# Performance work log

Measured on AMD Instinct MI355X. Metric: run time of the kernel, lower is better.

Reference implementation:

```python
import jax, jax.numpy as jnp
import numpy as np

N = 50000      # num nodes
E = 800000     # num edges (avg degree 16)
IN_FEA = 256
OU_FEA = 64


def setup_inputs() -> dict:
    key = jax.random.key(0)
    k_h, k_w, k_r, k_c, k_v = jax.random.split(key, 5)
    h = jax.random.normal(k_h, (N, IN_FEA), dtype=jnp.float32)
    # Linear(in_fea, ou_fea, bias=None): weight applied as h @ W, W [IN, OUT]
    W = jax.random.normal(k_w, (IN_FEA, OU_FEA), dtype=jnp.float32) / np.sqrt(IN_FEA)
    row = jax.random.randint(k_r, (E,), 0, N, dtype=jnp.int32)
    col = jax.random.randint(k_c, (E,), 0, N, dtype=jnp.int32)
    vals = jax.random.uniform(k_v, (E,), dtype=jnp.float32)
    return {"h": h, "W": W, "row": row, "col": col, "vals": vals}


def reference(h, W, row, col, vals):
    # dense projection: [N, IN] @ [IN, OUT] -> [N, OUT]
    hp = h @ W
    # torch builds sparse tensor with indices [col, row], i.e. G = A^T,
    # so torch.sparse.mm(G, hp)[i] = sum over edges with col==i of vals * hp[row]
    msg = hp[row] * vals[:, None]                      # [E, OUT] gather + scale
    out = jax.ops.segment_sum(msg, col, num_segments=N)  # scatter-add to dest
    return out
```

## Files before the change

### kernel.cpp

```cpp
#include <hip/hip_runtime.h>
#include <hip/hip_bf16.h>

#define IN_F 256
#define OU_F 64
#define BKN 128
#define BSHIFT 7
#define CHUNK 4096
#define STAGE_CAP 4096

typedef __attribute__((ext_vector_type(8))) short short8;
typedef __attribute__((ext_vector_type(4))) float f32x4;

__device__ inline short8 cvt8(float4 a, float4 b)
{
    union { short8 s8; __hip_bfloat162 h2[4]; } u;
    u.h2[0] = __float22bfloat162_rn(make_float2(a.x, a.y));
    u.h2[1] = __float22bfloat162_rn(make_float2(a.z, a.w));
    u.h2[2] = __float22bfloat162_rn(make_float2(b.x, b.y));
    u.h2[3] = __float22bfloat162_rn(make_float2(b.z, b.w));
    return u.s8;
}

__global__ void __launch_bounds__(256, 4)
gemm_mfma_kernel(const float* __restrict__ h, const float* __restrict__ W,
                 float* __restrict__ hp, int N)
{
    __shared__ unsigned short Wt[64][264];
    const int t = threadIdx.x;

#pragma unroll
    for (int i = 0; i < 32; ++i) {
        int p  = t + i * 256;
        int c  = p & 63;
        int k0 = (p >> 6) << 1;
        float x = W[(size_t)k0 * OU_F + c];
        float y = W[(size_t)(k0 + 1) * OU_F + c];
        __hip_bfloat162 bb = __float22bfloat162_rn(make_float2(x, y));
        *reinterpret_cast<unsigned*>(&Wt[c][k0]) = *reinterpret_cast<unsigned*>(&bb);
    }
    __syncthreads();

    const int l    = t & 63;
    const int wv   = t >> 6;
    const int cl   = l & 15;
    const int kg   = l >> 4;
    const int rbase = blockIdx.x * 64 + wv * 16;
    const int r    = rbase + cl;
    const int rld  = min(r, N - 1);
    const float4* hrow = reinterpret_cast<const float4*>(h) + (size_t)rld * (IN_F / 4);

    f32x4 acc[4];
#pragma unroll
    for (int nt = 0; nt < 4; ++nt) acc[nt] = (f32x4){0.f, 0.f, 0.f, 0.f};

#pragma unroll
    for (int ks = 0; ks < 8; ++ks) {
        float4 a0 = hrow[ks * 8 + kg * 2];
        float4 a1 = hrow[ks * 8 + kg * 2 + 1];
        short8 af = cvt8(a0, a1);
#pragma unroll
        for (int nt = 0; nt < 4; ++nt) {
            short8 bf = *reinterpret_cast<const short8*>(&Wt[nt * 16 + cl][ks * 32 + kg * 8]);
            acc[nt] = __builtin_amdgcn_mfma_f32_16x16x32_bf16(af, bf, acc[nt], 0, 0, 0);
        }
    }

#pragma unroll
    for (int nt = 0; nt < 4; ++nt)
#pragma unroll
        for (int rg = 0; rg < 4; ++rg) {
            int rr = rbase + kg * 4 + rg;
            if (rr < N)
                hp[(size_t)rr * OU_F + nt * 16 + cl] = acc[nt][rg];
        }
}

__global__ void __launch_bounds__(256)
hist_kernel(const int* __restrict__ col, int* __restrict__ bcnt, int E, int NB)
{
    __shared__ int lh[512];
    const int t = threadIdx.x;
    lh[t] = 0; lh[t + 256] = 0;
    __syncthreads();
    const int n4 = E >> 2;
    const int4* c4 = (const int4*)col;
    for (int i = blockIdx.x * 256 + t; i < n4; i += gridDim.x * 256) {
        int4 v = c4[i];
        atomicAdd(&lh[v.x >> BSHIFT], 1);
        atomicAdd(&lh[v.y >> BSHIFT], 1);
        atomicAdd(&lh[v.z >> BSHIFT], 1);
        atomicAdd(&lh[v.w >> BSHIFT], 1);
    }
    if (blockIdx.x == 0)
        for (int e = (n4 << 2) + t; e < E; e += 256)
            atomicAdd(&lh[col[e] >> BSHIFT], 1);
    __syncthreads();
    for (int i = t; i < NB; i += 256)
        if (lh[i]) atomicAdd(&bcnt[i], lh[i]);
}

__global__ void __launch_bounds__(256)
scan_kernel(const int* __restrict__ bcnt, int* __restrict__ boffs,
            int* __restrict__ bcursor, int NB)
{
    __shared__ int c[512];
    __shared__ int s[256];
    const int t = threadIdx.x;
    c[t]       = (t < NB)       ? bcnt[t] : 0;
    c[t + 256] = (t + 256 < NB) ? bcnt[t + 256] : 0;
    __syncthreads();
    s[t] = c[2 * t] + c[2 * t + 1];
    __syncthreads();
    for (int d = 1; d < 256; d <<= 1) {
        int v = (t >= d) ? s[t - d] : 0;
        __syncthreads();
        s[t] += v;
        __syncthreads();
    }
    int excl = (t > 0) ? s[t - 1] : 0;
    int e0 = excl;
    int e1 = excl + c[2 * t];
    if (2 * t < NB)     { boffs[2 * t]     = e0; bcursor[2 * t]     = e0; }
    if (2 * t + 1 < NB) { boffs[2 * t + 1] = e1; bcursor[2 * t + 1] = e1; }
    if (t == 255) boffs[NB] = s[255];
}

__global__ void __launch_bounds__(256)
partition_kernel(const int* __restrict__ row, const int* __restrict__ col,
                 const float* __restrict__ vals, int* __restrict__ bcursor,
                 int2* __restrict__ epk, int E, int NB)
{
    __shared__ int  hist[512];
    __shared__ int  X[512];
    __shared__ int  gshift[512];
    __shared__ int  s[256];
    __shared__ int2 stage[CHUNK];
    __shared__ int  gpos[CHUNK];

    const int t = threadIdx.x;
    const int base = blockIdx.x * CHUNK;
    const int n = min(CHUNK, E - base);

    hist[t] = 0; hist[t + 256] = 0;
    __syncthreads();

#pragma unroll
    for (int k = 0; k < 16; ++k) {
        int i = t + k * 256;
        if (i < n) atomicAdd(&hist[col[base + i] >> BSHIFT], 1);
    }
    __syncthreads();

    s[t] = hist[2 * t] + hist[2 * t + 1];
    __syncthreads();
    for (int d = 1; d < 256; d <<= 1) {
        int v = (t >= d) ? s[t - d] : 0;
        __syncthreads();
        s[t] += v;
        __syncthreads();
    }
    int excl = (t > 0) ? s[t - 1] : 0;
    X[2 * t]     = excl;
    X[2 * t + 1] = excl + hist[2 * t];
    __syncthreads();

    for (int i = t; i < NB; i += 256) {
        int hcnt = hist[i];
        int g = hcnt ? atomicAdd(&bcursor[i], hcnt) : 0;
        gshift[i] = g - X[i];
    }
    __syncthreads();

#pragma unroll
    for (int k = 0; k < 16; ++k) {
        int i = t + k * 256;
        if (i < n) {
            int e  = base + i;
            int cv = col[e];
            int b  = cv >> BSHIFT;
            int r  = atomicAdd(&X[b], 1);
            unsigned pk = (unsigned)row[e] | ((unsigned)(cv & (BKN - 1)) << 17);
            stage[r] = make_int2((int)pk, __float_as_int(vals[e]));
            gpos[r]  = gshift[b] + r;
        }
    }
    __syncthreads();

#pragma unroll
    for (int k = 0; k < 16; ++k) {
        int i = t + k * 256;
        if (i < n) epk[gpos[i]] = stage[i];
    }
}

__global__ void __launch_bounds__(256)
csr_kernel(const int2* __restrict__ epk, const int* __restrict__ boffs,
           int2* __restrict__ epk2, int* __restrict__ node_offs,
           int N, int NB)
{
    __shared__ int  cnt[BKN];
    __shared__ int  sc[BKN];
    __shared__ int  cur[BKN];
    __shared__ int2 stage[STAGE_CAP];
    const int t = threadIdx.x;
    const int b = blockIdx.x;
    const int s = boffs[b], e = boffs[b + 1];
    const int n = e - s;
    const int node0 = b << BSHIFT;

    if (t < BKN) cnt[t] = 0;
    __syncthreads();
    for (int i = t; i < n; i += 256)
        atomicAdd(&cnt[((unsigned)epk[s + i].x) >> 17], 1);
    __syncthreads();

    if (t < BKN) sc[t] = cnt[t];
    __syncthreads();
    for (int d = 1; d < BKN; d <<= 1) {
        int v = 0;
        if (t < BKN && t >= d) v = sc[t - d];
        __syncthreads();
        if (t < BKN) sc[t] += v;
        __syncthreads();
    }
    if (t < BKN) {
        int excl = sc[t] - cnt[t];
        cur[t] = excl;
        int node = node0 + t;
        if (node < N) node_offs[node] = s + excl;
    }
    if (b == NB - 1 && t == 0) node_offs[N] = e;
    __syncthreads();

    if (n <= STAGE_CAP) {
        for (int i = t; i < n; i += 256) {
            int2 r = epk[s + i];
            int pos = atomicAdd(&cur[((unsigned)r.x) >> 17], 1);
            stage[pos] = r;
        }
        __syncthreads();
        for (int i = t; i < n; i += 256)
            epk2[s + i] = stage[i];
    } else {
        for (int i = t; i < n; i += 256) {
            int2 r = epk[s + i];
            int pos = atomicAdd(&cur[((unsigned)r.x) >> 17], 1);
            epk2[s + pos] = r;
        }
    }
}

__global__ void __launch_bounds__(256)
gather_kernel(const float* __restrict__ hp, const int* __restrict__ node_offs,
              const int2* __restrict__ epk2, float* __restrict__ out, int N)
{
    int wid  = (int)((blockIdx.x * 256u + threadIdx.x) >> 6);
    int lane = threadIdx.x & 63;
    if (wid >= N) return;
    int s = node_offs[wid], e = node_offs[wid + 1];
    float acc = 0.f;
    for (int base = s; base < e; base += 64) {
        int n = min(64, e - base);
        int2 m = make_int2(0, 0);
        if (lane < n) m = epk2[base + lane];
        int j = 0;
        for (; j + 4 <= n; j += 4) {
            unsigned r0 = (unsigned)__shfl(m.x, j)     & 0x1FFFFu;
            unsigned r1 = (unsigned)__shfl(m.x, j + 1) & 0x1FFFFu;
            unsigned r2 = (unsigned)__shfl(m.x, j + 2) & 0x1FFFFu;
            unsigned r3 = (unsigned)__shfl(m.x, j + 3) & 0x1FFFFu;
            float v0 = __int_as_float(__shfl(m.y, j));
            float v1 = __int_as_float(__shfl(m.y, j + 1));
            float v2 = __int_as_float(__shfl(m.y, j + 2));
            float v3 = __int_as_float(__shfl(m.y, j + 3));
            float x0 = hp[((size_t)r0 << 6) + lane];
            float x1 = hp[((size_t)r1 << 6) + lane];
            float x2 = hp[((size_t)r2 << 6) + lane];
            float x3 = hp[((size_t)r3 << 6) + lane];
            acc = fmaf(v0, x0, acc);
            acc = fmaf(v1, x1, acc);
            acc = fmaf(v2, x2, acc);
            acc = fmaf(v3, x3, acc);
        }
        for (; j < n; ++j) {
            unsigned r = (unsigned)__shfl(m.x, j) & 0x1FFFFu;
            float    v = __int_as_float(__shfl(m.y, j));
            acc = fmaf(v, hp[((size_t)r << 6) + lane], acc);
        }
    }
    out[(size_t)wid * OU_F + lane] = acc;
}

__global__ void __launch_bounds__(256)
scatter_kernel(const float* __restrict__ hp, const int* __restrict__ row,
               const int* __restrict__ col, const float* __restrict__ vals,
               float* __restrict__ out, int E)
{
    unsigned int gid = blockIdx.x * 256u + threadIdx.x;
    int e = (int)(gid >> 6);
    if (e >= E) return;
    int f = (int)(gid & 63u);
    int r = row[e], c = col[e];
    float m = vals[e] * hp[(size_t)r * OU_F + f];
    __hip_atomic_fetch_add(&out[(size_t)c * OU_F + f], m,
                           __ATOMIC_RELAXED, __HIP_MEMORY_SCOPE_AGENT);
}

extern "C" void kernel_launch(void* const* d_in, const int* in_sizes, int n_in,
                              void* d_out, int out_size, void* d_ws, size_t ws_size,
                              hipStream_t stream)
{
    const float* h    = (const float*)d_in[0];
    const float* W    = (const float*)d_in[1];
    const int*   row  = (const int*)d_in[2];
    const int*   col  = (const int*)d_in[3];
    const float* vals = (const float*)d_in[4];
    float*       out  = (float*)d_out;

    const int N = in_sizes[0] / IN_F;
    const int E = in_sizes[2];
    const int NB = (N + BKN - 1) / BKN;

    char*  ws  = (char*)d_ws;
    size_t off = 0;
    auto alloc = [&](size_t bytes) -> char* {
        char* p = ws + off;
        off = (off + bytes + 255) & ~(size_t)255;
        return p;
    };
    float* hp        = (float*)alloc((size_t)N * OU_F * 4);
    int*   bcnt      = (int*)  alloc((size_t)NB * 4);
    int*   boffs     = (int*)  alloc((size_t)(NB + 1) * 4);
    int*   bcursor   = (int*)  alloc((size_t)NB * 4);
    int*   node_offs = (int*)  alloc((size_t)(N + 1) * 4);
    int2*  epk       = (int2*) alloc((size_t)E * 8);
    int2*  epk2      = (int2*) alloc((size_t)E * 8);
    const bool fits = (off <= ws_size) && (NB <= 512) && (N < 131072);

    const int ntiles = (N + 63) / 64;
    gemm_mfma_kernel<<<ntiles, 256, 0, stream>>>(h, W, hp, N);

    if (fits) {
        hipMemsetAsync(bcnt, 0, (size_t)NB * 4, stream);
        hist_kernel<<<256, 256, 0, stream>>>(col, bcnt, E, NB);
        scan_kernel<<<1, 256, 0, stream>>>(bcnt, boffs, bcursor, NB);
        partition_kernel<<<(E + CHUNK - 1) / CHUNK, 256, 0, stream>>>(
            row, col, vals, bcursor, epk, E, NB);
        csr_kernel<<<NB, 256, 0, stream>>>(epk, boffs, epk2, node_offs, N, NB);
        gather_kernel<<<(N + 3) / 4, 256, 0, stream>>>(hp, node_offs, epk2, out, N);
    } else {
        hipMemsetAsync(d_out, 0, (size_t)out_size * sizeof(float), stream);
        unsigned long long total = (unsigned long long)E * 64ull;
        unsigned int sgrid = (unsigned int)((total + 255ull) / 256ull);
        scatter_kernel<<<sgrid, 256, 0, stream>>>(hp, row, col, vals, out, E);
    }
}
```

Before: 89.98 us.

## Store projected features as bf16, stage h tile in LDS, shrink partition chunk

The projected feature matrix hp is now written in bf16 instead of fp32. This halves its footprint and the bytes moved by the random row gathers in the gather and scatter kernels. The GEMM now converts the whole 64-row h tile to bf16 into swizzled shared memory with coalesced loads before running the MFMA loop, and drops the occupancy hint. The partition kernel chunk shrinks from 4096 to 1024 edges to launch more blocks and use less shared memory per block. The trade-off is extra rounding in hp, which adds error to the aggregated output.

New measurement: 97.51 us. 8.4% more time.

```diff
diff --git a/kernel.cpp b/kernel.cpp
--- a/kernel.cpp
+++ b/kernel.cpp
@@ -5,27 +5,19 @@
 #define OU_F 64
 #define BKN 128
 #define BSHIFT 7
-#define CHUNK 4096
+#define CHUNK 1024
 #define STAGE_CAP 4096
 
 typedef __attribute__((ext_vector_type(8))) short short8;
 typedef __attribute__((ext_vector_type(4))) float f32x4;
 
-__device__ inline short8 cvt8(float4 a, float4 b)
-{
-    union { short8 s8; __hip_bfloat162 h2[4]; } u;
-    u.h2[0] = __float22bfloat162_rn(make_float2(a.x, a.y));
-    u.h2[1] = __float22bfloat162_rn(make_float2(a.z, a.w));
-    u.h2[2] = __float22bfloat162_rn(make_float2(b.x, b.y));
-    u.h2[3] = __float22bfloat162_rn(make_float2(b.z, b.w));
-    return u.s8;
-}
-
-__global__ void __launch_bounds__(256, 4)
+__global__ void __launch_bounds__(256)
 gemm_mfma_kernel(const float* __restrict__ h, const float* __restrict__ W,
-                 float* __restrict__ hp, int N)
+                 __hip_bfloat16* __restrict__ hp, int N)
 {
     __shared__ unsigned short Wt[64][264];
+    __shared__ uint4 hsv[2048];
+    unsigned char* hs = reinterpret_cast<unsigned char*>(hsv);
     const int t = threadIdx.x;
 
 #pragma unroll
@@ -38,16 +30,32 @@
         __hip_bfloat162 bb = __float22bfloat162_rn(make_float2(x, y));
         *reinterpret_cast<unsigned*>(&Wt[c][k0]) = *reinterpret_cast<unsigned*>(&bb);
     }
+
+    const int rbase = blockIdx.x * 64;
+    const int nrow  = min(64, N - rbase);
+#pragma unroll
+    for (int i = 0; i < 16; ++i) {
+        int idx = t + i * 256;
+        int r  = idx >> 6;
+        int k4 = idx & 63;
+        float4 v = make_float4(0.f, 0.f, 0.f, 0.f);
+        if (r < nrow)
+            v = reinterpret_cast<const float4*>(h)[(size_t)(rbase + r) * (IN_F / 4) + k4];
+        __hip_bfloat162 lo = __float22bfloat162_rn(make_float2(v.x, v.y));
+        __hip_bfloat162 hi = __float22bfloat162_rn(make_float2(v.z, v.w));
+        unsigned boff = (unsigned)r * 512u + (((unsigned)k4 * 8u) ^ (((unsigned)r & 7u) << 4));
+        uint2 pk;
+        pk.x = *reinterpret_cast<unsigned*>(&lo);
+        pk.y = *reinterpret_cast<unsigned*>(&hi);
+        *reinterpret_cast<uint2*>(&hs[boff]) = pk;
+    }
     __syncthreads();
 
     const int l    = t & 63;
     const int wv   = t >> 6;
     const int cl   = l & 15;
     const int kg   = l >> 4;
-    const int rbase = blockIdx.x * 64 + wv * 16;
-    const int r    = rbase + cl;
-    const int rld  = min(r, N - 1);
-    const float4* hrow = reinterpret_cast<const float4*>(h) + (size_t)rld * (IN_F / 4);
+    const int rloc = wv * 16 + cl;
 
     f32x4 acc[4];
 #pragma unroll
@@ -55,9 +63,9 @@
 
 #pragma unroll
     for (int ks = 0; ks < 8; ++ks) {
-        float4 a0 = hrow[ks * 8 + kg * 2];
-        float4 a1 = hrow[ks * 8 + kg * 2 + 1];
-        short8 af = cvt8(a0, a1);
+        unsigned aoff = (unsigned)rloc * 512u +
+                        (((unsigned)(ks * 64 + kg * 16)) ^ (((unsigned)rloc & 7u) << 4));
+        short8 af = *reinterpret_cast<const short8*>(&hs[aoff]);
 #pragma unroll
         for (int nt = 0; nt < 4; ++nt) {
             short8 bf = *reinterpret_cast<const short8*>(&Wt[nt * 16 + cl][ks * 32 + kg * 8]);
@@ -69,9 +77,9 @@
     for (int nt = 0; nt < 4; ++nt)
 #pragma unroll
         for (int rg = 0; rg < 4; ++rg) {
-            int rr = rbase + kg * 4 + rg;
+            int rr = rbase + wv * 16 + kg * 4 + rg;
             if (rr < N)
-                hp[(size_t)rr * OU_F + nt * 16 + cl] = acc[nt][rg];
+                hp[(size_t)rr * OU_F + nt * 16 + cl] = __float2bfloat16(acc[nt][rg]);
         }
 }
 
@@ -145,7 +153,7 @@
     __syncthreads();
 
 #pragma unroll
-    for (int k = 0; k < 16; ++k) {
+    for (int k = 0; k < CHUNK / 256; ++k) {
         int i = t + k * 256;
         if (i < n) atomicAdd(&hist[col[base + i] >> BSHIFT], 1);
     }
@@ -172,7 +180,7 @@
     __syncthreads();
 
 #pragma unroll
-    for (int k = 0; k < 16; ++k) {
+    for (int k = 0; k < CHUNK / 256; ++k) {
         int i = t + k * 256;
         if (i < n) {
             int e  = base + i;
@@ -187,7 +195,7 @@
     __syncthreads();
 
 #pragma unroll
-    for (int k = 0; k < 16; ++k) {
+    for (int k = 0; k < CHUNK / 256; ++k) {
         int i = t + k * 256;
         if (i < n) epk[gpos[i]] = stage[i];
     }
@@ -251,7 +259,7 @@
 }
 
 __global__ void __launch_bounds__(256)
-gather_kernel(const float* __restrict__ hp, const int* __restrict__ node_offs,
+gather_kernel(const __hip_bfloat16* __restrict__ hp, const int* __restrict__ node_offs,
               const int2* __restrict__ epk2, float* __restrict__ out, int N)
 {
     int wid  = (int)((blockIdx.x * 256u + threadIdx.x) >> 6);
@@ -273,10 +281,10 @@
             float v1 = __int_as_float(__shfl(m.y, j + 1));
             float v2 = __int_as_float(__shfl(m.y, j + 2));
             float v3 = __int_as_float(__shfl(m.y, j + 3));
-            float x0 = hp[((size_t)r0 << 6) + lane];
-            float x1 = hp[((size_t)r1 << 6) + lane];
-            float x2 = hp[((size_t)r2 << 6) + lane];
-            float x3 = hp[((size_t)r3 << 6) + lane];
+            float x0 = __bfloat162float(hp[((size_t)r0 << 6) + lane]);
+            float x1 = __bfloat162float(hp[((size_t)r1 << 6) + lane]);
+            float x2 = __bfloat162float(hp[((size_t)r2 << 6) + lane]);
+            float x3 = __bfloat162float(hp[((size_t)r3 << 6) + lane]);
             acc = fmaf(v0, x0, acc);
             acc = fmaf(v1, x1, acc);
             acc = fmaf(v2, x2, acc);
@@ -285,14 +293,14 @@
         for (; j < n; ++j) {
             unsigned r = (unsigned)__shfl(m.x, j) & 0x1FFFFu;
             float    v = __int_as_float(__shfl(m.y, j));
-            acc = fmaf(v, hp[((size_t)r << 6) + lane], acc);
+            acc = fmaf(v, __bfloat162float(hp[((size_t)r << 6) + lane]), acc);
         }
     }
     out[(size_t)wid * OU_F + lane] = acc;
 }
 
 __global__ void __launch_bounds__(256)
-scatter_kernel(const float* __restrict__ hp, const int* __restrict__ row,
+scatter_kernel(const __hip_bfloat16* __restrict__ hp, const int* __restrict__ row,
                const int* __restrict__ col, const float* __restrict__ vals,
                float* __restrict__ out, int E)
 {
@@ -301,7 +309,7 @@
     if (e >= E) return;
     int f = (int)(gid & 63u);
     int r = row[e], c = col[e];
-    float m = vals[e] * hp[(size_t)r * OU_F + f];
+    float m = vals[e] * __bfloat162float(hp[(size_t)r * OU_F + f]);
     __hip_atomic_fetch_add(&out[(size_t)c * OU_F + f], m,
                            __ATOMIC_RELAXED, __HIP_MEMORY_SCOPE_AGENT);
 }
@@ -328,7 +336,7 @@
         off = (off + bytes + 255) & ~(size_t)255;
         return p;
     };
-    float* hp        = (float*)alloc((size_t)N * OU_F * 4);
+    __hip_bfloat16* hp = (__hip_bfloat16*)alloc((size_t)N * OU_F * 2);
     int*   bcnt      = (int*)  alloc((size_t)NB * 4);
     int*   boffs     = (int*)  alloc((size_t)(NB + 1) * 4);
     int*   bcursor   = (int*)  alloc((size_t)NB * 4);
```
